# Kernel optimization log

Measured on AMD Instinct MI355X. Metric: run time of the kernel, lower is better.

Reference implementation:

```python
import jax, jax.numpy as jnp
import numpy as np

D_MODEL = 256
B, T = 4, 96
NLIN = 3
# 3-point Gauss-Legendre nodes mapped from [-1,1] to [0,1]: 0.5*(1 +/- sqrt(3/5)), 0.5
GAUSS_NODES = jnp.array([0.1127016653792583, 0.5, 0.8872983346207417], dtype=jnp.float32)
# weights as hard-coded in the torch module (gauss_weight[3])
GAUSS_W = jnp.array([0.55555, 0.88888, 0.55555], dtype=jnp.float32)


def setup_inputs() -> dict:
    key = jax.random.key(0)
    ks = jax.random.split(key, 8)
    s = 1.0 / np.sqrt(D_MODEL)
    return {
        "x": jax.random.normal(ks[0], (B, T, D_MODEL), dtype=jnp.float32),
        "t": jax.random.uniform(ks[1], (B, T), dtype=jnp.float32),
        # ConcatLinear_v2 layer 1: Linear(D,D) + hyper_bias Linear(1,D,no bias)
        "W1": jax.random.normal(ks[2], (D_MODEL, D_MODEL), dtype=jnp.float32) * s,
        "b1": jnp.zeros((D_MODEL,), dtype=jnp.float32),
        "u1": jax.random.normal(ks[3], (D_MODEL,), dtype=jnp.float32) * s,
        # ConcatLinear_v2 layer 2
        "W2": jax.random.normal(ks[4], (D_MODEL, D_MODEL), dtype=jnp.float32) * s,
        "b2": jnp.zeros((D_MODEL,), dtype=jnp.float32),
        "u2": jax.random.normal(ks[5], (D_MODEL,), dtype=jnp.float32) * s,
    }


def _ode_forward(x, t, W1, b1, u1, W2, b2, u2):
    Bv, Tv, D = x.shape
    # pairwise expansion: row index = query q (target time t1), col index = key j (start time t0)
    x0 = jnp.broadcast_to(x[:, None, :, :], (Bv, Tv, Tv, D)).reshape(-1, D)   # [N, D]
    t0 = jnp.broadcast_to(t[:, None, :], (Bv, Tv, Tv)).reshape(-1)            # [N]
    t1 = jnp.broadcast_to(t[:, :, None], (Bv, Tv, Tv)).reshape(-1)            # [N]
    ratio = (t1 - t0)[:, None]                                                # (end-start)/(1-0)

    def odefunc(tt, y):
        # ConcatLinear_v2: y @ W.T + b + t * u, softplus between layers
        h = jax.nn.softplus(y @ W1.T + b1 + tt[:, None] * u1)
        return h @ W2.T + b2 + tt[:, None] * u2

    def f(s, y):
        # time reparameterization s in [0,1] -> t = t0 + s*(t1-t0); dy/ds = (t1-t0)*func(t,y)
        tt = t0 + s * (t1 - t0)
        return odefunc(tt, y) * ratio

    ss = jnp.concatenate([jnp.zeros((1,), dtype=jnp.float32), GAUSS_NODES])

    def step(y, s_pair):
        s0, s1 = s_pair
        dt = s1 - s0
        third = jnp.float32(1.0 / 3.0)
        # torchdiffeq fixed-grid rk4 (3/8 rule)
        k1 = f(s0, y)
        k2 = f(s0 + dt * third, y + dt * k1 * third)
        k3 = f(s0 + dt * 2 * third, y + dt * (k2 - k1 * third))
        k4 = f(s1, y + dt * (k1 - k2 + k3))
        y1 = y + (k1 + 3 * (k2 + k3) + k4) * dt * 0.125
        return y1, y1

    _, ys = jax.lax.scan(step, x0, (ss[:-1], ss[1:]))  # [K=3, N, D]
    y = ys.reshape(NLIN, Bv, Tv, Tv, D).transpose(1, 2, 3, 0, 4)  # [B, Q, T, K, D]
    y = y * (GAUSS_W * 0.5)[None, None, None, :, None]
    return y


def reference(x, t, W1, b1, u1, W2, b2, u2):
    return _ode_forward(x, t, W1, b1, u1, W2, b2, u2)
```

## Files before the change

kernel.cpp:

```cpp
#include <hip/hip_runtime.h>
#include <hip/hip_fp16.h>

typedef float f32x4 __attribute__((ext_vector_type(4)));
typedef float f32x2 __attribute__((ext_vector_type(2)));
typedef _Float16 f16x8 __attribute__((ext_vector_type(8)));
typedef __fp16 fp16x2 __attribute__((ext_vector_type(2)));

#define T_LEN 96
#define DM    256
#define NSAMP 32
#define MT 2
#define NT 2
#define BUF_USH 8192
#define LDS_TOTAL 32768

__device__ __forceinline__ float softplus_f(float x){
    float u = __expf(-fabsf(x));
    return fmaxf(x, 0.f) + __logf(1.0f + u);
}
__device__ __forceinline__ uint pkrtz(float a, float b){
    fp16x2 h = __builtin_amdgcn_cvt_pkrtz(a, b);
    return *(uint*)&h;
}
__device__ __forceinline__ f32x2 pk_add(f32x2 a, f32x2 b){
    f32x2 d; asm("v_pk_add_f32 %0, %1, %2" : "=v"(d) : "v"(a), "v"(b)); return d;
}
__device__ __forceinline__ f32x2 pk_mul(f32x2 a, f32x2 b){
    f32x2 d; asm("v_pk_mul_f32 %0, %1, %2" : "=v"(d) : "v"(a), "v"(b)); return d;
}
__device__ __forceinline__ f32x2 pk_fma(f32x2 a, f32x2 b, f32x2 c){
    f32x2 d; asm("v_pk_fma_f32 %0, %1, %2, %3" : "=v"(d) : "v"(a), "v"(b), "v"(c)); return d;
}
__device__ __forceinline__ f32x2 lo2(f32x4 v){ return __builtin_shufflevector(v, v, 0, 1); }
__device__ __forceinline__ f32x2 hi2(f32x4 v){ return __builtin_shufflevector(v, v, 2, 3); }
__device__ __forceinline__ f32x2 bc2(float s){ return (f32x2){s, s}; }

__global__ void pack_w_kernel(const float* __restrict__ W1, const float* __restrict__ W2,
                              ushort* __restrict__ ws){
    int idx = blockIdx.x*256 + threadIdx.x;
    const float* W = blockIdx.y ? W2 : W1;
    ushort* dst = ws + (size_t)blockIdx.y*65536;
    float w = W[idx];
    int d = idx >> 8, k = idx & 255;
    int off = ((((d>>4)<<3) + (k>>5))<<9) + (((d&15) | (((k>>3)&3)<<4))<<3) + (k&7);
    dst[off] = __half_as_ushort(__float2half_rn(w));
}

__global__ __launch_bounds__(512)
void ode_mfma_kernel(const float* __restrict__ x, const float* __restrict__ t,
                     const float* __restrict__ b1, const float* __restrict__ u1,
                     const float* __restrict__ b2, const float* __restrict__ u2,
                     const ushort* __restrict__ wpk, float* __restrict__ out)
{
    __shared__ __align__(16) ushort ylds[LDS_TOTAL];

    const int tid  = threadIdx.x;
    const int wvd  = tid >> 6;
    const int lane = tid & 63;
    const int l15  = lane & 15;
    const int l4   = lane >> 4;
    const int base = blockIdx.x * NSAMP;

    f16x8 W1f[MT][8], W2f[MT][8];
#pragma unroll
    for(int mt=0; mt<MT; mt++)
#pragma unroll
        for(int ks=0; ks<8; ks++){
            const int off = ((((2*wvd+mt)<<3)+ks)<<9) + (lane<<3);
            W1f[mt][ks] = *(const f16x8*)(wpk + off);
            W2f[mt][ks] = *(const f16x8*)(wpk + 65536 + off);
        }

    float t0v[NT], rat[NT];
    f32x2 rat2[NT];
    f32x2 y[MT][NT][2], k1[MT][NT][2], k2[MT][NT][2];
    f32x4 acc[MT][NT];

    f32x2 B2h[MT][2], U2h[MT][2];
#pragma unroll
    for(int mt=0; mt<MT; mt++){
        const int db = 32*wvd + mt*16 + l4*4;
        f32x4 b2v = *(const f32x4*)(b2 + db);
        f32x4 u2v = *(const f32x4*)(u2 + db);
        B2h[mt][0]=lo2(b2v); B2h[mt][1]=hi2(b2v);
        U2h[mt][0]=lo2(u2v); U2h[mt][1]=hi2(u2v);
    }

    int pofs[MT][NT];
#pragma unroll
    for(int mt=0; mt<MT; mt++)
#pragma unroll
        for(int nt=0; nt<NT; nt++){
            int row = nt*16 + l15;
            int gs  = (4*wvd + 2*mt + (l4>>1)) ^ (row & 7);
            pofs[mt][nt] = row*256 + gs*8 + (l4&1)*4;
        }

    int vb[NT];
#pragma unroll
    for(int nt=0; nt<NT; nt++){
        int row = nt*16 + l15;
        vb[nt] = row*512 + ((l4 ^ (row&3))*16) + ((row&4)*16);
    }

#pragma unroll
    for(int nt=0; nt<NT; nt++){
        int n = base + nt*16 + l15;
        int b = n / (T_LEN*T_LEN);
        int r = n - b*(T_LEN*T_LEN);
        int q = r / T_LEN;
        int j = r - q*T_LEN;
        float ta = t[b*T_LEN + j], tb = t[b*T_LEN + q];
        t0v[nt] = ta; rat[nt] = tb - ta; rat2[nt] = bc2(tb - ta);
        const float* xr = x + (size_t)(b*T_LEN + j)*DM;
#pragma unroll
        for(int mt=0; mt<MT; mt++){
            const int db = 32*wvd + mt*16 + l4*4;
            f32x4 v = *(const f32x4*)(xr + db);
            y[mt][nt][0] = lo2(v); y[mt][nt][1] = hi2(v);
        }
    }

    auto put = [&](int idx, f32x2 v01, f32x2 v23){
        uint p0 = pkrtz(v01[0], v01[1]), p1 = pkrtz(v23[0], v23[1]);
        *(uint2*)&ylds[idx] = make_uint2(p0, p1);
    };

    auto matmul = [&](const f16x8 (&Wf)[MT][8], int buf){
        const char* bb = (const char*)ylds + (buf<<14);
        __builtin_amdgcn_s_setprio(1);
#pragma unroll
        for(int mt=0; mt<MT; mt++)
#pragma unroll
            for(int nt=0; nt<NT; nt++)
                acc[mt][nt] = (f32x4){0.f,0.f,0.f,0.f};
#pragma unroll
        for(int ks=0; ks<8; ks++){
#pragma unroll
            for(int nt=0; nt<NT; nt++){
                f16x8 bh = *(const f16x8*)(bb + (vb[nt] ^ (ks<<6)));
#pragma unroll
                for(int mt=0; mt<MT; mt++)
                    acc[mt][nt] = __builtin_amdgcn_mfma_f32_16x16x32_f16(Wf[mt][ks], bh, acc[mt][nt], 0,0,0);
            }
        }
        __builtin_amdgcn_s_setprio(0);
    };

    auto hidden = [&](const f32x2* tt2){
#pragma unroll
        for(int mt=0; mt<MT; mt++){
            const int db = 32*wvd + mt*16 + l4*4;
            f32x4 bv = *(const f32x4*)(b1 + db);
            f32x4 uv = *(const f32x4*)(u1 + db);
            f32x2 bp[2] = {lo2(bv), hi2(bv)}, up[2] = {lo2(uv), hi2(uv)};
#pragma unroll
            for(int nt=0; nt<NT; nt++){
                f32x2 v[2];
#pragma unroll
                for(int p=0;p<2;p++){
                    f32x2 ap = p ? hi2(acc[mt][nt]) : lo2(acc[mt][nt]);
                    f32x2 s  = pk_fma(tt2[nt], up[p], pk_add(ap, bp[p]));
                    v[p] = (f32x2){ softplus_f(s[0]), softplus_f(s[1]) };
                }
                put(BUF_USH + pofs[mt][nt], v[0], v[1]);
            }
        }
    };

#pragma unroll
    for(int mt=0; mt<MT; mt++)
#pragma unroll
        for(int nt=0; nt<NT; nt++)
            put(pofs[mt][nt], y[mt][nt][0], y[mt][nt][1]);
    __syncthreads();

    const f32x2 neg1 = bc2(-1.f), four2 = bc2(4.f), three2 = bc2(3.f);

    float s0 = 0.f;
#pragma unroll 1
    for(int step=0; step<3; step++){
        const float s1 = (step==0) ? 0.1127016653792583f : ((step==1) ? 0.5f : 0.8872983346207417f);
        const float gw = ((step==1) ? 0.88888f : 0.55555f) * 0.5f;
        const float dt = s1 - s0;
        const float c3 = dt * (1.f/3.f);
        const f32x2 dt2 = bc2(dt), c32 = bc2(c3), nc32 = bc2(-c3), dt82 = bc2(dt*0.125f);
        const f32x2 gw2 = bc2(gw);
        f32x2 tt2[NT];

#pragma unroll
        for(int nt=0; nt<NT; nt++) tt2[nt] = bc2(t0v[nt] + s0*rat[nt]);
        matmul(W1f, 0);
        hidden(tt2);
        __syncthreads();
        matmul(W2f, 1);

#pragma unroll
        for(int mt=0; mt<MT; mt++)
#pragma unroll
            for(int nt=0; nt<NT; nt++){
                f32x2 v[2];
#pragma unroll
                for(int p=0;p<2;p++){
                    f32x2 ap = p ? hi2(acc[mt][nt]) : lo2(acc[mt][nt]);
                    f32x2 kk = pk_mul(pk_fma(tt2[nt], U2h[mt][p], pk_add(ap, B2h[mt][p])), rat2[nt]);
                    k1[mt][nt][p] = kk;
                    v[p] = pk_fma(c32, kk, y[mt][nt][p]);
                }
                put(pofs[mt][nt], v[0], v[1]);
            }
        __syncthreads();

#pragma unroll
        for(int nt=0; nt<NT; nt++) tt2[nt] = bc2(t0v[nt] + (s0+c3)*rat[nt]);
        matmul(W1f, 0);
        hidden(tt2);
        __syncthreads();
        matmul(W2f, 1);

#pragma unroll
        for(int mt=0; mt<MT; mt++)
#pragma unroll
            for(int nt=0; nt<NT; nt++){
                f32x2 v[2];
#pragma unroll
                for(int p=0;p<2;p++){
                    f32x2 ap = p ? hi2(acc[mt][nt]) : lo2(acc[mt][nt]);
                    f32x2 kk = pk_mul(pk_fma(tt2[nt], U2h[mt][p], pk_add(ap, B2h[mt][p])), rat2[nt]);
                    f32x2 k1o = k1[mt][nt][p];
                    v[p] = pk_fma(dt2, kk, pk_fma(nc32, k1o, y[mt][nt][p]));
                    k1[mt][nt][p] = pk_fma(kk, neg1, k1o);
                    k2[mt][nt][p] = kk;
                }
                put(pofs[mt][nt], v[0], v[1]);
            }
        __syncthreads();

#pragma unroll
        for(int nt=0; nt<NT; nt++) tt2[nt] = bc2(t0v[nt] + (s0+2.f*c3)*rat[nt]);
        matmul(W1f, 0);
        hidden(tt2);
        __syncthreads();
        matmul(W2f, 1);

#pragma unroll
        for(int mt=0; mt<MT; mt++)
#pragma unroll
            for(int nt=0; nt<NT; nt++){
                f32x2 v[2];
#pragma unroll
                for(int p=0;p<2;p++){
                    f32x2 ap = p ? hi2(acc[mt][nt]) : lo2(acc[mt][nt]);
                    f32x2 k3v = pk_mul(pk_fma(tt2[nt], U2h[mt][p], pk_add(ap, B2h[mt][p])), rat2[nt]);
                    f32x2 d12 = k1[mt][nt][p];
                    v[p] = pk_fma(dt2, pk_add(d12, k3v), y[mt][nt][p]);
                    f32x2 inner = pk_fma(four2, k2[mt][nt][p], pk_fma(three2, k3v, d12));
                    y[mt][nt][p] = pk_fma(dt82, inner, y[mt][nt][p]);
                }
                put(pofs[mt][nt], v[0], v[1]);
            }
        __syncthreads();

#pragma unroll
        for(int nt=0; nt<NT; nt++) tt2[nt] = bc2(t0v[nt] + s1*rat[nt]);
        matmul(W1f, 0);
        hidden(tt2);
        __syncthreads();
        matmul(W2f, 1);

        {
            float* yf = (float*)&ylds[2*BUF_USH];
#pragma unroll
            for(int mt=0; mt<MT; mt++)
#pragma unroll
                for(int nt=0; nt<NT; nt++){
                    const int row = nt*16 + l15;
                    f32x4 ov;
#pragma unroll
                    for(int p=0;p<2;p++){
                        f32x2 ap = p ? hi2(acc[mt][nt]) : lo2(acc[mt][nt]);
                        f32x2 k4v = pk_mul(pk_fma(tt2[nt], U2h[mt][p], pk_add(ap, B2h[mt][p])), rat2[nt]);
                        f32x2 yn  = pk_fma(dt82, k4v, y[mt][nt][p]);
                        y[mt][nt][p] = yn;
                        f32x2 o = pk_mul(yn, gw2);
                        ov[2*p] = o[0]; ov[2*p+1] = o[1];
                    }
                    put(pofs[mt][nt], y[mt][nt][0], y[mt][nt][1]);
                    const int c = 8*wvd + 4*mt + l4;
                    const int p2 = c ^ (row & 7);
                    *(f32x4*)&yf[row*256 + p2*4] = ov;
                }
            __syncthreads();
#pragma unroll
            for(int i=0;i<4;i++){
                const int r = 4*wvd + i;
                f32x4 v = *(const f32x4*)&yf[r*256 + ((lane ^ (r&7))&63)*4];
                __builtin_nontemporal_store(v,
                    (f32x4*)(out + ((size_t)(base + r)*3 + step)*DM + lane*4));
            }
        }
        s0 = s1;
    }
}

extern "C" void kernel_launch(void* const* d_in, const int* in_sizes, int n_in,
                              void* d_out, int out_size, void* d_ws, size_t ws_size,
                              hipStream_t stream)
{
    const float* x  = (const float*)d_in[0];
    const float* t  = (const float*)d_in[1];
    const float* W1 = (const float*)d_in[2];
    const float* b1 = (const float*)d_in[3];
    const float* u1 = (const float*)d_in[4];
    const float* W2 = (const float*)d_in[5];
    const float* b2 = (const float*)d_in[6];
    const float* u2 = (const float*)d_in[7];
    ushort* wpk = (ushort*)d_ws;

    pack_w_kernel<<<dim3(256,2), 256, 0, stream>>>(W1, W2, wpk);
    ode_mfma_kernel<<<dim3((4*T_LEN*T_LEN)/NSAMP), 512, 0, stream>>>(
        x, t, b1, u1, b2, u2, wpk, (float*)d_out);
}
```

Measured before the change: 197.8 us.

## Double samples per block and keep RK state as packed fp16 in registers

```diff
diff --git a/kernel.cpp b/kernel.cpp
--- a/kernel.cpp
+++ b/kernel.cpp
@@ -8,11 +8,11 @@
 
 #define T_LEN 96
 #define DM    256
-#define NSAMP 32
+#define NSAMP 64
 #define MT 2
-#define NT 2
-#define BUF_USH 8192
-#define LDS_TOTAL 32768
+#define NT 4
+#define BUF_USH 16384
+#define LDS_TOTAL 65536
 
 __device__ __forceinline__ float softplus_f(float x){
     float u = __expf(-fabsf(x));
@@ -21,6 +21,11 @@
 __device__ __forceinline__ uint pkrtz(float a, float b){
     fp16x2 h = __builtin_amdgcn_cvt_pkrtz(a, b);
     return *(uint*)&h;
+}
+__device__ __forceinline__ uint pk2(f32x2 v){ return pkrtz(v[0], v[1]); }
+__device__ __forceinline__ f32x2 up2(uint u){
+    return (f32x2){ __half2float(__ushort_as_half((ushort)(u & 0xffffu))),
+                    __half2float(__ushort_as_half((ushort)(u >> 16))) };
 }
 __device__ __forceinline__ f32x2 pk_add(f32x2 a, f32x2 b){
     f32x2 d; asm("v_pk_add_f32 %0, %1, %2" : "=v"(d) : "v"(a), "v"(b)); return d;
@@ -72,18 +77,17 @@
         }
 
     float t0v[NT], rat[NT];
-    f32x2 rat2[NT];
-    f32x2 y[MT][NT][2], k1[MT][NT][2], k2[MT][NT][2];
+    uint yp[MT][NT][2], k1p[MT][NT][2], k2p[MT][NT][2];
     f32x4 acc[MT][NT];
 
-    f32x2 B2h[MT][2], U2h[MT][2];
+    uint B2p[MT][2], U2p[MT][2];
 #pragma unroll
     for(int mt=0; mt<MT; mt++){
         const int db = 32*wvd + mt*16 + l4*4;
         f32x4 b2v = *(const f32x4*)(b2 + db);
         f32x4 u2v = *(const f32x4*)(u2 + db);
-        B2h[mt][0]=lo2(b2v); B2h[mt][1]=hi2(b2v);
-        U2h[mt][0]=lo2(u2v); U2h[mt][1]=hi2(u2v);
+        B2p[mt][0]=pk2(lo2(b2v)); B2p[mt][1]=pk2(hi2(b2v));
+        U2p[mt][0]=pk2(lo2(u2v)); U2p[mt][1]=pk2(hi2(u2v));
     }
 
     int pofs[MT][NT];
@@ -102,6 +106,10 @@
         int row = nt*16 + l15;
         vb[nt] = row*512 + ((l4 ^ (row&3))*16) + ((row&4)*16);
     }
+
+    auto put = [&](int idx, f32x2 v01, f32x2 v23){
+        *(uint2*)&ylds[idx] = make_uint2(pk2(v01), pk2(v23));
+    };
 
 #pragma unroll
     for(int nt=0; nt<NT; nt++){
@@ -111,23 +119,19 @@
         int q = r / T_LEN;
         int j = r - q*T_LEN;
         float ta = t[b*T_LEN + j], tb = t[b*T_LEN + q];
-        t0v[nt] = ta; rat[nt] = tb - ta; rat2[nt] = bc2(tb - ta);
+        t0v[nt] = ta; rat[nt] = tb - ta;
         const float* xr = x + (size_t)(b*T_LEN + j)*DM;
 #pragma unroll
         for(int mt=0; mt<MT; mt++){
             const int db = 32*wvd + mt*16 + l4*4;
             f32x4 v = *(const f32x4*)(xr + db);
-            y[mt][nt][0] = lo2(v); y[mt][nt][1] = hi2(v);
+            yp[mt][nt][0] = pk2(lo2(v)); yp[mt][nt][1] = pk2(hi2(v));
+            put(pofs[mt][nt], lo2(v), hi2(v));
         }
     }
 
-    auto put = [&](int idx, f32x2 v01, f32x2 v23){
-        uint p0 = pkrtz(v01[0], v01[1]), p1 = pkrtz(v23[0], v23[1]);
-        *(uint2*)&ylds[idx] = make_uint2(p0, p1);
-    };
-
     auto matmul = [&](const f16x8 (&Wf)[MT][8], int buf){
-        const char* bb = (const char*)ylds + (buf<<14);
+        const char* bb = (const char*)ylds + (buf<<15);
         __builtin_amdgcn_s_setprio(1);
 #pragma unroll
         for(int mt=0; mt<MT; mt++)
@@ -168,11 +172,6 @@
         }
     };
 
-#pragma unroll
-    for(int mt=0; mt<MT; mt++)
-#pragma unroll
-        for(int nt=0; nt<NT; nt++)
-            put(pofs[mt][nt], y[mt][nt][0], y[mt][nt][1]);
     __syncthreads();
 
     const f32x2 neg1 = bc2(-1.f), four2 = bc2(4.f), three2 = bc2(3.f);
@@ -203,9 +202,9 @@
 #pragma unroll
                 for(int p=0;p<2;p++){
                     f32x2 ap = p ? hi2(acc[mt][nt]) : lo2(acc[mt][nt]);
-                    f32x2 kk = pk_mul(pk_fma(tt2[nt], U2h[mt][p], pk_add(ap, B2h[mt][p])), rat2[nt]);
-                    k1[mt][nt][p] = kk;
-                    v[p] = pk_fma(c32, kk, y[mt][nt][p]);
+                    f32x2 kk = pk_mul(pk_fma(tt2[nt], up2(U2p[mt][p]), pk_add(ap, up2(B2p[mt][p]))), bc2(rat[nt]));
+                    k1p[mt][nt][p] = pk2(kk);
+                    v[p] = pk_fma(c32, kk, up2(yp[mt][nt][p]));
                 }
                 put(pofs[mt][nt], v[0], v[1]);
             }
@@ -226,11 +225,11 @@
 #pragma unroll
                 for(int p=0;p<2;p++){
                     f32x2 ap = p ? hi2(acc[mt][nt]) : lo2(acc[mt][nt]);
-                    f32x2 kk = pk_mul(pk_fma(tt2[nt], U2h[mt][p], pk_add(ap, B2h[mt][p])), rat2[nt]);
-                    f32x2 k1o = k1[mt][nt][p];
-                    v[p] = pk_fma(dt2, kk, pk_fma(nc32, k1o, y[mt][nt][p]));
-                    k1[mt][nt][p] = pk_fma(kk, neg1, k1o);
-                    k2[mt][nt][p] = kk;
+                    f32x2 kk = pk_mul(pk_fma(tt2[nt], up2(U2p[mt][p]), pk_add(ap, up2(B2p[mt][p]))), bc2(rat[nt]));
+                    f32x2 k1o = up2(k1p[mt][nt][p]);
+                    v[p] = pk_fma(dt2, kk, pk_fma(nc32, k1o, up2(yp[mt][nt][p])));
+                    k1p[mt][nt][p] = pk2(pk_fma(kk, neg1, k1o));
+                    k2p[mt][nt][p] = pk2(kk);
                 }
                 put(pofs[mt][nt], v[0], v[1]);
             }
@@ -251,11 +250,12 @@
 #pragma unroll
                 for(int p=0;p<2;p++){
                     f32x2 ap = p ? hi2(acc[mt][nt]) : lo2(acc[mt][nt]);
-                    f32x2 k3v = pk_mul(pk_fma(tt2[nt], U2h[mt][p], pk_add(ap, B2h[mt][p])), rat2[nt]);
-                    f32x2 d12 = k1[mt][nt][p];
-                    v[p] = pk_fma(dt2, pk_add(d12, k3v), y[mt][nt][p]);
-                    f32x2 inner = pk_fma(four2, k2[mt][nt][p], pk_fma(three2, k3v, d12));
-                    y[mt][nt][p] = pk_fma(dt82, inner, y[mt][nt][p]);
+                    f32x2 k3v = pk_mul(pk_fma(tt2[nt], up2(U2p[mt][p]), pk_add(ap, up2(B2p[mt][p]))), bc2(rat[nt]));
+                    f32x2 d12 = up2(k1p[mt][nt][p]);
+                    f32x2 yo  = up2(yp[mt][nt][p]);
+                    v[p] = pk_fma(dt2, pk_add(d12, k3v), yo);
+                    f32x2 inner = pk_fma(four2, up2(k2p[mt][nt][p]), pk_fma(three2, k3v, d12));
+                    yp[mt][nt][p] = pk2(pk_fma(dt82, inner, yo));
                 }
                 put(pofs[mt][nt], v[0], v[1]);
             }
@@ -276,24 +276,26 @@
                 for(int nt=0; nt<NT; nt++){
                     const int row = nt*16 + l15;
                     f32x4 ov;
+                    f32x2 yn0, yn1;
 #pragma unroll
                     for(int p=0;p<2;p++){
                         f32x2 ap = p ? hi2(acc[mt][nt]) : lo2(acc[mt][nt]);
-                        f32x2 k4v = pk_mul(pk_fma(tt2[nt], U2h[mt][p], pk_add(ap, B2h[mt][p])), rat2[nt]);
-                        f32x2 yn  = pk_fma(dt82, k4v, y[mt][nt][p]);
-                        y[mt][nt][p] = yn;
+                        f32x2 k4v = pk_mul(pk_fma(tt2[nt], up2(U2p[mt][p]), pk_add(ap, up2(B2p[mt][p]))), bc2(rat[nt]));
+                        f32x2 yn  = pk_fma(dt82, k4v, up2(yp[mt][nt][p]));
+                        yp[mt][nt][p] = pk2(yn);
+                        if(p==0) yn0 = yn; else yn1 = yn;
                         f32x2 o = pk_mul(yn, gw2);
                         ov[2*p] = o[0]; ov[2*p+1] = o[1];
                     }
-                    put(pofs[mt][nt], y[mt][nt][0], y[mt][nt][1]);
+                    put(pofs[mt][nt], yn0, yn1);
                     const int c = 8*wvd + 4*mt + l4;
                     const int p2 = c ^ (row & 7);
                     *(f32x4*)&yf[row*256 + p2*4] = ov;
                 }
             __syncthreads();
 #pragma unroll
-            for(int i=0;i<4;i++){
-                const int r = 4*wvd + i;
+            for(int i=0;i<8;i++){
+                const int r = 8*wvd + i;
                 f32x4 v = *(const f32x4*)&yf[r*256 + ((lane ^ (r&7))&63)*4];
                 __builtin_nontemporal_store(v,
                     (f32x4*)(out + ((size_t)(base + r)*3 + step)*DM + lane*4));
```

After: 394.9 us. 2x slower.
